# Performance work log

Hardware: AMD Instinct MI355X
Metric: run time of the kernel (lower is better)

## Reference

```python
import jax, jax.numpy as jnp
import numpy as np

B, T_ENC, T_DEC = 16, 256, 200
E, ATT, PRE, H, MEL, LOC, K = 512, 128, 256, 1024, 80, 32, 31


def setup_inputs() -> dict:
    key = jax.random.key(0)
    ks = jax.random.split(key, 20)
    s = lambda k, shape: jax.random.normal(k, shape, jnp.float32) * 0.02
    return dict(
        encoder_output=jax.random.normal(ks[0], (B, T_ENC, E), jnp.float32),
        padded_mels=jax.random.normal(ks[1], (B, T_DEC, MEL), jnp.float32),
        enc_proj_w=s(ks[2], (ATT, E)),
        lstm_proj_w=s(ks[3], (ATT, H)),
        loc_conv_w=s(ks[4], (LOC, 1, K)),
        loc_conv_b=jnp.zeros((LOC,), jnp.float32),
        loc_dense_w=s(ks[5], (ATT, LOC)),
        loc_dense_b=jnp.zeros((ATT,), jnp.float32),
        e_w=s(ks[6], (1, ATT)),
        e_b=jnp.zeros((1,), jnp.float32),
        prenet1_w=s(ks[7], (PRE, MEL)),
        prenet2_w=s(ks[8], (PRE, PRE)),
        w_ih0=s(ks[9], (4 * H, PRE + E)),
        w_hh0=s(ks[10], (4 * H, H)),
        b_ih0=jnp.zeros((4 * H,), jnp.float32),
        b_hh0=jnp.zeros((4 * H,), jnp.float32),
        w_ih1=s(ks[11], (4 * H, H)),
        w_hh1=s(ks[12], (4 * H, H)),
        b_ih1=jnp.zeros((4 * H,), jnp.float32),
        b_hh1=jnp.zeros((4 * H,), jnp.float32),
        proj_w=s(ks[13], (MEL, H + E)),
        proj_b=jnp.zeros((MEL,), jnp.float32),
        stop_w=s(ks[14], (1, H + E)),
        stop_b=jnp.zeros((1,), jnp.float32),
        text_lengths=jax.random.randint(ks[15], (B,), T_ENC // 2, T_ENC + 1),
    )


def _lstm_cell_zero(x, w_ih, b_ih, b_hh):
    # PyTorch LSTM cell with zero initial (h, c): h_prev contributes nothing
    # except the recurrent bias b_hh. Gate order: i, f, g, o.
    g = x @ w_ih.T + b_ih + b_hh
    i, f, gg, o = jnp.split(g, 4, axis=-1)
    c = jax.nn.sigmoid(i) * jnp.tanh(gg)  # f * c_prev == 0
    return jax.nn.sigmoid(o) * jnp.tanh(c)


def reference(encoder_output, padded_mels, enc_proj_w, lstm_proj_w, loc_conv_w,
              loc_conv_b, loc_dense_w, loc_dense_b, e_w, e_b, prenet1_w,
              prenet2_w, w_ih0, w_hh0, b_ih0, b_hh0, w_ih1, w_hh1, b_ih1,
              b_hh1, proj_w, proj_b, stop_w, stop_b, text_lengths):
    b, t_enc, _ = encoder_output.shape
    n_mel = padded_mels.shape[-1]
    h = w_hh0.shape[-1]
    pad = (loc_conv_w.shape[-1] - 1) // 2
    proc_enc = encoder_output @ enc_proj_w.T              # [B,Te,128]
    mask = jnp.arange(t_enc)[None, :] < text_lengths[:, None]
    # teacher forcing (ratio=1.0): prev mel at step t is padded_mels[:, t-1]
    prev_mels = jnp.concatenate(
        [jnp.zeros((b, 1, n_mel), padded_mels.dtype), padded_mels[:, :-1]],
        axis=1).transpose(1, 0, 2)                        # [Td,B,80]

    def step(carry, prev_mel):
        awc, h2 = carry                                   # [B,Te], [B,1024]
        # prenet (dropout omitted for a deterministic reference)
        x = jax.nn.relu(prev_mel @ prenet1_w.T)
        x = jax.nn.relu(x @ prenet2_w.T)                  # [B,256]
        # location-sensitive attention
        q = h2 @ lstm_proj_w.T                            # [B,128]
        loc = jax.lax.conv_general_dilated(
            awc[:, None, :], loc_conv_w, (1,), [(pad, pad)],
            dimension_numbers=('NCH', 'OIH', 'NCH')) + loc_conv_b[None, :, None]
        loc = jnp.einsum('bct,ac->bta', loc, loc_dense_w) + loc_dense_b
        en = jnp.tanh(q[:, None, :] + loc + proc_enc) @ e_w[0] + e_b[0]
        en = jnp.where(mask, en, -1e9)
        aw = jax.nn.softmax(en, axis=-1)                  # [B,Te]
        ctx = jnp.einsum('bt,bte->be', aw, encoder_output)  # [B,512]
        # 2-layer LSTM, state reset to zero every step (as in the original)
        li = jnp.concatenate([x, ctx], axis=-1)           # [B,768]
        h1 = _lstm_cell_zero(li, w_ih0, b_ih0, b_hh0)
        h2n = _lstm_cell_zero(h1, w_ih1, b_ih1, b_hh1)
        dec = jnp.concatenate([h2n, ctx], axis=-1)        # [B,1536]
        mel = dec @ proj_w.T + proj_b                     # [B,80]
        stop = (dec @ stop_w.T + stop_b)[:, 0]            # [B]
        return (awc + aw, h2n), (mel, stop)

    init = (jnp.zeros((b, t_enc), encoder_output.dtype),
            jnp.zeros((b, h), encoder_output.dtype))
    _, (mels, stops) = jax.lax.scan(step, init, prev_mels)
    return mels.transpose(1, 0, 2), stops.T               # [B,Td,80], [B,Td]
```

## Files before the change

kernel.cpp:

```cpp
#include <hip/hip_runtime.h>
#include <math.h>

#define NB   16
#define TE   256
#define TD   200
#define EE   512
#define ATT  128
#define PREN 256
#define HH   1024
#define NMEL 80
#define NLOC 32
#define KWW  31
#define PADW 15

#define OFF_X2H  0
#define OFF_PE   (OFF_X2H + TD*NB*128)
#define OFF_ENR  (OFF_PE + NB*TE*ATT)
#define OFF_CTR  (OFF_ENR + NB*16*6*4)
#define OFF_H1H  (OFF_CTR + NB*128*4)
#define OFF_H2R  (OFF_H1H + NB*512)
#define OFF_QVR  (OFF_H2R + NB*256*4)
#define OFF_BAR  (OFF_QVR + NB*16*2*4)
#define BAR_U32  4096
#define ARR_G 0

#define LW0X_U32 (12*128)
#define LW0C_U32 (12*256)
#define LW1_U32  (12*512)
#define DYN_BYTES ((LW0X_U32 + LW0C_U32 + LW1_U32)*4)

typedef float f4 __attribute__((ext_vector_type(4)));
typedef unsigned int u32x4 __attribute__((ext_vector_type(4)));
typedef unsigned int u32x2 __attribute__((ext_vector_type(2)));
typedef _Float16 h2t __attribute__((ext_vector_type(2)));

__device__ __forceinline__ float fast_sigm(float x) { return 1.0f / (1.0f + __expf(-x)); }
__device__ __forceinline__ float fast_tanh(float x) { return 1.0f - 2.0f / (__expf(2.0f*x) + 1.0f); }
__device__ __forceinline__ float dot4(f4 a, f4 b) {
  return a.x*b.x + a.y*b.y + a.z*b.z + a.w*b.w;
}
__device__ __forceinline__ float red32(float v) {
  v += __shfl_down(v, 16, 32); v += __shfl_down(v, 8, 32);
  v += __shfl_down(v, 4, 32);  v += __shfl_down(v, 2, 32);
  v += __shfl_down(v, 1, 32);
  return v;
}
__device__ __forceinline__ float red64(float v) {
  v += __shfl_down(v, 32); v += __shfl_down(v, 16); v += __shfl_down(v, 8);
  v += __shfl_down(v, 4);  v += __shfl_down(v, 2);  v += __shfl_down(v, 1);
  return v;
}
__device__ __forceinline__ float fdot2(unsigned a, unsigned b, float c) {
  return __builtin_amdgcn_fdot2(__builtin_bit_cast(h2t, a),
                                __builtin_bit_cast(h2t, b), c, false);
}
__device__ __forceinline__ unsigned pkh(float a, float b) {
  h2t h; h.x = (_Float16)a; h.y = (_Float16)b;
  return __builtin_bit_cast(unsigned, h);
}
__device__ __forceinline__ float hlo(unsigned u) {
  return (float)__builtin_bit_cast(h2t, u).x;
}
__device__ __forceinline__ float hhi(unsigned u) {
  return (float)__builtin_bit_cast(h2t, u).y;
}

__device__ __forceinline__ unsigned ld_cg_u32(const unsigned* p) {
  unsigned r;
  asm volatile("global_load_dword %0, %1, off sc0 sc1\n\ts_waitcnt vmcnt(0)"
               : "=v"(r) : "v"(p) : "memory");
  return r;
}
__device__ __forceinline__ void st_cg_u32(unsigned* p, unsigned v) {
  asm volatile("global_store_dword %0, %1, off sc0 sc1" :: "v"(p), "v"(v) : "memory");
}
__device__ __forceinline__ f4 ld_cg_f4(const f4* p) {
  f4 r;
  asm volatile("global_load_dwordx4 %0, %1, off sc0 sc1\n\ts_waitcnt vmcnt(0)"
               : "=v"(r) : "v"(p) : "memory");
  return r;
}
__device__ __forceinline__ void st_cg_f4(f4* p, f4 v) {
  asm volatile("global_store_dwordx4 %0, %1, off sc0 sc1" :: "v"(p), "v"(v) : "memory");
}
__device__ __forceinline__ u32x4 ld_cg_u4(const void* p) {
  u32x4 r;
  asm volatile("global_load_dwordx4 %0, %1, off sc0 sc1\n\ts_waitcnt vmcnt(0)"
               : "=v"(r) : "v"(p) : "memory");
  return r;
}
__device__ __forceinline__ void st_cg_u4(void* p, u32x4 v) {
  asm volatile("global_store_dwordx4 %0, %1, off sc0 sc1" :: "v"(p), "v"(v) : "memory");
}
__device__ __forceinline__ void st_cg_u2(void* p, u32x2 v) {
  asm volatile("global_store_dwordx2 %0, %1, off sc0 sc1" :: "v"(p), "v"(v) : "memory");
}
__device__ __forceinline__ f4 ld_l2_f4(const f4* p) {
  f4 r;
  asm volatile("global_load_dwordx4 %0, %1, off sc0\n\ts_waitcnt vmcnt(0)"
               : "=v"(r) : "v"(p) : "memory");
  return r;
}
__device__ __forceinline__ void st_l2_f4(f4* p, f4 v) {
  asm volatile("global_store_dwordx4 %0, %1, off sc0" :: "v"(p), "v"(v) : "memory");
}
__device__ __forceinline__ u32x4 ld_l2_u4(const void* p) {
  u32x4 r;
  asm volatile("global_load_dwordx4 %0, %1, off sc0\n\ts_waitcnt vmcnt(0)"
               : "=v"(r) : "v"(p) : "memory");
  return r;
}
__device__ __forceinline__ void st_l2_u4(void* p, u32x4 v) {
  asm volatile("global_store_dwordx4 %0, %1, off sc0" :: "v"(p), "v"(v) : "memory");
}
__device__ __forceinline__ void ld4u(u32x4& a, u32x4& b, u32x4& c, u32x4& d,
                                     const void* pa, const void* pb,
                                     const void* pc, const void* pd) {
  asm volatile(
    "global_load_dwordx4 %0, %4, off sc0 sc1\n\t"
    "global_load_dwordx4 %1, %5, off sc0 sc1\n\t"
    "global_load_dwordx4 %2, %6, off sc0 sc1\n\t"
    "global_load_dwordx4 %3, %7, off sc0 sc1\n\t"
    "s_waitcnt vmcnt(0)"
    : "=&v"(a), "=&v"(b), "=&v"(c), "=&v"(d)
    : "v"(pa), "v"(pb), "v"(pc), "v"(pd) : "memory");
}

__device__ __forceinline__ void g_arrive(unsigned* bar, unsigned e) {
  __syncthreads();
  if (threadIdx.x == 0) st_cg_u32(bar + ARR_G + blockIdx.x * 16, e);
}
__device__ __forceinline__ void g_wait(unsigned* bar, unsigned e) {
  if (threadIdx.x < 256) {
    while (ld_cg_u32(bar + ARR_G + threadIdx.x * 16) < e) {}
  }
  __syncthreads();
}

__global__ void k_init(float* __restrict__ ws) {
  const int gid = blockIdx.x * 256 + threadIdx.x;
  f4* enr = (f4*)(ws + OFF_ENR);
  u32x4* ctr = (u32x4*)(ws + OFF_CTR);
  f4* h2r = (f4*)(ws + OFF_H2R);
  f4* qvr = (f4*)(ws + OFF_QVR);
  unsigned* bar = (unsigned*)(ws + OFF_BAR);
  const f4 z = (f4){0.f, 0.f, 0.f, 0.f};
  const u32x4 zu = (u32x4){0u, 0u, 0u, 0u};
  for (int i = gid; i < NB*16*6; i += 32*256) st_cg_f4(enr + i, z);
  for (int i = gid; i < NB*128; i += 32*256) st_cg_u4(ctr + i, zu);
  for (int i = gid; i < NB*256; i += 32*256) st_cg_f4(h2r + i, z);
  for (int i = gid; i < NB*32; i += 32*256) st_cg_f4(qvr + i, z);
  for (int i = gid; i < BAR_U32; i += 32*256) st_cg_u32(bar + i, 0u);
}

__global__ void k_prenet(const float* __restrict__ mels,
                         const float* __restrict__ w1,
                         const float* __restrict__ w2,
                         float* __restrict__ ws) {
  const int t = blockIdx.x >> 4;
  const int b = blockIdx.x & 15;
  const int j = threadIdx.x;
  __shared__ float s_in[NMEL];
  __shared__ float s_x1[PREN];
  if (j < NMEL) s_in[j] = (t == 0) ? 0.0f : mels[(b*TD + (t-1))*NMEL + j];
  __syncthreads();
  float a1 = 0.0f;
  #pragma unroll 8
  for (int k = 0; k < NMEL; ++k) a1 += s_in[k] * w1[j*NMEL + k];
  s_x1[j] = fmaxf(a1, 0.0f);
  __syncthreads();
  float a2 = 0.0f;
  #pragma unroll 8
  for (int k = 0; k < PREN; ++k) a2 += s_x1[k] * w2[j*PREN + k];
  ((_Float16*)(ws + OFF_X2H))[((size_t)t*NB + b)*256 + j] = (_Float16)fmaxf(a2, 0.0f);
}

__global__ void k_procenc(const float* __restrict__ enc,
                          const float* __restrict__ w,
                          float* __restrict__ pe) {
  const int bt = blockIdx.x;
  const int a = threadIdx.x;
  __shared__ float s_e[EE];
  for (int k = a; k < EE; k += 128) s_e[k] = enc[bt*EE + k];
  __syncthreads();
  float acc = 0.0f;
  #pragma unroll 8
  for (int k = 0; k < EE; ++k) acc += s_e[k] * w[a*EE + k];
  pe[bt*ATT + a] = acc;
}

__global__ void __launch_bounds__(512, 1) k_main(
    const float* __restrict__ enc,
    const float* __restrict__ lstm_proj_w,
    const float* __restrict__ loc_conv_w,
    const float* __restrict__ loc_conv_b,
    const float* __restrict__ loc_dense_w,
    const float* __restrict__ loc_dense_b,
    const float* __restrict__ e_w,
    const float* __restrict__ e_b,
    const float* __restrict__ w_ih0,
    const float* __restrict__ b_ih0,
    const float* __restrict__ b_hh0,
    const float* __restrict__ w_ih1,
    const float* __restrict__ b_ih1,
    const float* __restrict__ b_hh1,
    const float* __restrict__ proj_w,
    const float* __restrict__ proj_b,
    const float* __restrict__ stop_w,
    const float* __restrict__ stop_b,
    const int*   __restrict__ text_len,
    float* __restrict__ ws,
    float* __restrict__ out) {
  const int bid = blockIdx.x;
  const int tid = threadIdx.x;

  const unsigned* x2h = (const unsigned*)(ws + OFF_X2H);
  float* pe  = ws + OFF_PE;
  f4* en_rec = (f4*)(ws + OFF_ENR);
  u32x4* ct_rec = (u32x4*)(ws + OFF_CTR);
  unsigned* h1h = (unsigned*)(ws + OFF_H1H);
  f4* h2_rec = (f4*)(ws + OFF_H2R);
  f4* qv_rec = (f4*)(ws + OFF_QVR);
  unsigned* bar = (unsigned*)(ws + OFF_BAR);

  __shared__ __align__(16) float s_ldw[NLOC*ATT];
  __shared__ float s_awcf[TE];
  __shared__ float s_loc[16*33];
  __shared__ float s_red[16];
  __shared__ float s_en[256];
  __shared__ float s_aw[256];
  __shared__ float s_entmp[16];
  __shared__ float s_qtmp[8];
  __shared__ float s_ctmp[32];
  __shared__ __align__(16) float s_q[ATT];
  __shared__ __align__(16) float s_dec[HH+EE];
  __shared__ float s_b0[12], s_b1[12];
  extern __shared__ __align__(16) unsigned dynlds_u[];
  unsigned* lw0x = dynlds_u;
  unsigned* lw0c = lw0x + LW0X_U32;
  unsigned* lw1  = lw0c + LW0C_U32;

  const int b_grp = bid & 15;
  const int sub   = bid >> 4;
  const int h0    = bid * 4;

  for (int i = tid; i < NLOC*ATT; i += 512) {
    int c = i >> 7, a = i & 127;
    s_ldw[i] = loc_dense_w[a*NLOC + c];
  }
  if (tid < 12) {
    int g = tid >> 2, h = tid & 3;
    int gr = (g == 0 ? 0 : (g == 1 ? 2048 : 3072)) + h0 + h;
    s_b0[tid] = b_ih0[gr] + b_hh0[gr];
    s_b1[tid] = b_ih1[gr] + b_hh1[gr];
  }
  for (int i = tid; i < LW0X_U32; i += 512) {
    int r = i >> 7, c = i & 127;
    int g = r >> 2, h = r & 3;
    int grow = (g == 0 ? 0 : (g == 1 ? 2048 : 3072)) + h0 + h;
    const float* wr = w_ih0 + (size_t)grow*768;
    lw0x[i] = pkh(wr[2*c], wr[2*c+1]);
  }
  for (int i = tid; i < LW0C_U32; i += 512) {
    int r = i >> 8, c = i & 255;
    int g = r >> 2, h = r & 3;
    int grow = (g == 0 ? 0 : (g == 1 ? 2048 : 3072)) + h0 + h;
    const float* wr = w_ih0 + (size_t)grow*768 + 256;
    lw0c[i] = pkh(wr[2*c], wr[2*c+1]);
  }
  for (int i = tid; i < LW1_U32; i += 512) {
    int r = i >> 9, c = i & 511;
    int g = r >> 2, h = r & 3;
    int grow = (g == 0 ? 0 : (g == 1 ? 2048 : 3072)) + h0 + h;
    const float* wr = w_ih1 + (size_t)grow*1024;
    lw1[i] = pkh(wr[2*c], wr[2*c+1]);
  }
  if (tid < 256) s_awcf[tid] = 0.0f;

  const int   lenb = text_len[b_grp];
  const float eb0  = e_b[0];
  const int tl = tid >> 5;
  const int j  = tid & 31;
  float lcw_r[KWW];
  #pragma unroll
  for (int k = 0; k < KWW; ++k) lcw_r[k] = loc_conv_w[j*KWW + k];
  const float lcb_r = loc_conv_b[j];
  const f4 db_r = *(const f4*)(loc_dense_b + 4*j);
  const f4 ew_r = *(const f4*)(e_w + 4*j);
  const f4 pe_r = *(const f4*)(pe + (size_t)(b_grp*TE + sub*16 + tl)*ATT + 4*j);
  const f4 ps_r = pe_r + db_r;
  const int e4i = tid >> 6;
  const int ts  = tid & 63;
  f4 encr[4];
  {
    const f4* enc4 = (const f4*)(enc + (size_t)b_grp*TE*EE);
    #pragma unroll
    for (int i = 0; i < 4; ++i)
      encr[i] = enc4[(size_t)(ts + 64*i)*(EE/4) + sub*8 + e4i];
  }
  const int en_si = tid / 6;
  const int en_rr = tid - en_si*6;
  const f4* en_myrec = en_rec + (b_grp*16 + en_si)*6 + en_rr;
  const int pb = tid >> 5;
  const int kc = tid & 31;
  const u32x4* ct_my = ct_rec + pb*128;
  __syncthreads();

  unsigned eg = 0;

  for (int t = 0; t < TD; ++t) {
    const unsigned tg = (unsigned)(t + 1);
    f4 pre;
    {
      float cv = lcb_r;
      const int pos = sub*16 + tl;
      #pragma unroll
      for (int k = 0; k < KWW; ++k) {
        const int g = pos - PADW + k;
        const float av = (g >= 0 && g < TE) ? s_awcf[g] : 0.0f;
        cv += av * lcw_r[k];
      }
      s_loc[tl*33 + j] = cv;
      __syncthreads();
      f4 d4 = (f4){0.f, 0.f, 0.f, 0.f};
      #pragma unroll 8
      for (int c = 0; c < NLOC; ++c) {
        const float lv = s_loc[tl*33 + c];
        const f4 w4 = ((const f4*)s_ldw)[c*32 + j];
        d4.x += lv*w4.x; d4.y += lv*w4.y; d4.z += lv*w4.z; d4.w += lv*w4.w;
      }
      pre = ps_r + d4;
    }
    {
      if (tid < 32) {
        const int src = tid >> 1, r = tid & 1;
        const f4* qp = qv_rec + (b_grp*16 + src)*2 + r;
        f4 v = ld_l2_f4(qp);
        while (__float_as_uint(v.z) != (unsigned)t) v = ld_cg_f4(qp);
        const unsigned u0 = __float_as_uint(v.x), u1 = __float_as_uint(v.y);
        const int base = src*8 + r*4;
        s_q[base+0] = hlo(u0); s_q[base+1] = hhi(u0);
        s_q[base+2] = hlo(u1); s_q[base+3] = hhi(u1);
      }
      __syncthreads();
      const f4 q4 = *(const f4*)(s_q + 4*j);
      float acc = fast_tanh(pre.x+q4.x)*ew_r.x + fast_tanh(pre.y+q4.y)*ew_r.y
                + fast_tanh(pre.z+q4.z)*ew_r.z + fast_tanh(pre.w+q4.w)*ew_r.w;
      acc = red32(acc);
      if (j == 0) {
        float evv = acc + eb0;
        const int tt = sub*16 + tl;
        if (tt >= lenb) evv = -1e9f;
        s_entmp[tl] = evv;
      }
      __syncthreads();
      if (tid < 6) {
        f4 r = (f4){0.f, 0.f, 0.f, __uint_as_float(tg)};
        const int base = 3*tid;
        r.x = s_entmp[base];
        if (base + 1 < 16) r.y = s_entmp[base+1];
        if (base + 2 < 16) r.z = s_entmp[base+2];
        f4* dst = en_rec + (b_grp*16 + sub)*6 + tid;
        st_l2_f4(dst, r);
        st_cg_f4(dst, r);
      }
    }
    {
      if (tid < 96) {
        f4 v = ld_l2_f4(en_myrec);
        while (__float_as_uint(v.w) != tg) v = ld_cg_f4(en_myrec);
        const int base = en_si*16 + 3*en_rr;
        s_en[base] = v.x;
        if (3*en_rr + 1 < 16) s_en[base+1] = v.y;
        if (3*en_rr + 2 < 16) s_en[base+2] = v.z;
      } else if (t > 0 && tid >= 128 && tid < 320) {
        const int ol = (tid - 128) >> 5, kq = tid & 31;
        const int m = sub*6 + ol;
        if (m < 81) {
          const float* wrow = (m < NMEL) ? (proj_w + (size_t)m*(HH+EE)) : stop_w;
          const f4* w4 = (const f4*)wrow;
          const f4* s4 = (const f4*)s_dec;
          float a2 = 0.0f;
          #pragma unroll
          for (int i = 0; i < 12; ++i) a2 += dot4(s4[kq + 32*i], w4[kq + 32*i]);
          a2 = red32(a2);
          if (kq == 0) {
            if (m < NMEL) out[(b_grp*TD + (t-1))*NMEL + m] = a2 + proj_b[m];
            else          out[NB*TD*NMEL + b_grp*TD + (t-1)] = a2 + stop_b[0];
          }
        }
      }
      __syncthreads();
      float p = 0.f;
      if (tid < 256) {
        p = __expf(s_en[tid]);
        float sm = p;
        #pragma unroll
        for (int d = 32; d > 0; d >>= 1) sm += __shfl_xor(sm, d);
        if ((tid & 63) == 0) s_red[8 + (tid >> 6)] = sm;
      }
      __syncthreads();
      const float inv = 1.0f / (s_red[8] + s_red[9] + s_red[10] + s_red[11]);
      if (tid < 256) {
        const float aw = p * inv;
        s_aw[tid] = aw;
        s_awcf[tid] += aw;
      }
      __syncthreads();
      f4 a4 = (f4){0.f, 0.f, 0.f, 0.f};
      #pragma unroll
      for (int i = 0; i < 4; ++i) {
        const float awv = s_aw[ts + 64*i];
        a4.x += awv*encr[i].x; a4.y += awv*encr[i].y;
        a4.z += awv*encr[i].z; a4.w += awv*encr[i].w;
      }
      a4.x = red64(a4.x); a4.y = red64(a4.y); a4.z = red64(a4.z); a4.w = red64(a4.w);
      if (ts == 0) {
        s_ctmp[e4i*4+0] = a4.x; s_ctmp[e4i*4+1] = a4.y;
        s_ctmp[e4i*4+2] = a4.z; s_ctmp[e4i*4+3] = a4.w;
      }
      __syncthreads();
      if (tid < 8) {
        u32x4 w;
        w.x = pkh(s_ctmp[4*tid+0], s_ctmp[4*tid+1]);
        w.y = pkh(s_ctmp[4*tid+2], s_ctmp[4*tid+3]);
        w.z = tg; w.w = 0u;
        u32x4* dst = ct_rec + b_grp*128 + sub*8 + tid;
        st_l2_u4(dst, w);
        st_cg_u4(dst, w);
      }
    }
    float acc[12];
    {
      #pragma unroll
      for (int r = 0; r < 12; ++r) acc[r] = 0.0f;
      const u32x4 xv = ((const u32x4*)x2h)[((size_t)t*NB + pb)*32 + kc];
      #pragma unroll
      for (int r = 0; r < 12; ++r) {
        const u32x4 w = ((const u32x4*)lw0x)[r*32 + kc];
        acc[r] = fdot2(xv.x, w.x, acc[r]); acc[r] = fdot2(xv.y, w.y, acc[r]);
        acc[r] = fdot2(xv.z, w.z, acc[r]); acc[r] = fdot2(xv.w, w.w, acc[r]);
      }
    }
    {
      u32x4 ra, rb, rc, rd;
      for (;;) {
        ld4u(ra, rb, rc, rd, ct_my + 2*kc, ct_my + 2*kc + 1,
             ct_my + 2*kc + 64, ct_my + 2*kc + 65);
        if (ra.z == tg && rb.z == tg && rc.z == tg && rd.z == tg) break;
        __builtin_amdgcn_s_sleep(1);
      }
      const u32x4 c0 = (u32x4){ra.x, ra.y, rb.x, rb.y};
      const u32x4 c1 = (u32x4){rc.x, rc.y, rd.x, rd.y};
      #pragma unroll
      for (int r = 0; r < 12; ++r) {
        const u32x4 w0 = ((const u32x4*)lw0c)[r*64 + kc];
        const u32x4 w1 = ((const u32x4*)lw0c)[r*64 + kc + 32];
        acc[r] = fdot2(c0.x, w0.x, acc[r]); acc[r] = fdot2(c0.y, w0.y, acc[r]);
        acc[r] = fdot2(c0.z, w0.z, acc[r]); acc[r] = fdot2(c0.w, w0.w, acc[r]);
        acc[r] = fdot2(c1.x, w1.x, acc[r]); acc[r] = fdot2(c1.y, w1.y, acc[r]);
        acc[r] = fdot2(c1.z, w1.z, acc[r]); acc[r] = fdot2(c1.w, w1.w, acc[r]);
      }
      #pragma unroll
      for (int r = 0; r < 12; ++r) acc[r] = red32(acc[r]);
      if (kc == 0) {
        float hv[4];
        #pragma unroll
        for (int h = 0; h < 4; ++h) {
          const float gi = acc[h]   + s_b0[h];
          const float gg = acc[4+h] + s_b0[4+h];
          const float go = acc[8+h] + s_b0[8+h];
          hv[h] = fast_sigm(go) * fast_tanh(fast_sigm(gi) * fast_tanh(gg));
        }
        u32x2 stv; stv.x = pkh(hv[0], hv[1]); stv.y = pkh(hv[2], hv[3]);
        st_cg_u2((u32x2*)h1h + pb*256 + bid, stv);
      }
    }
    g_arrive(bar, ++eg);
    g_wait(bar, eg);
    {
      #pragma unroll
      for (int r = 0; r < 12; ++r) acc[r] = 0.0f;
      u32x4 v0, v1, v2, v3;
      const u32x4* hp = (const u32x4*)h1h + pb*128 + kc;
      ld4u(v0, v1, v2, v3, hp, hp+32, hp+64, hp+96);
      #pragma unroll
      for (int r = 0; r < 12; ++r) {
        const u32x4* wp = (const u32x4*)lw1 + r*128 + kc;
        const u32x4 w0 = wp[0], w1 = wp[32], w2 = wp[64], w3 = wp[96];
        acc[r] = fdot2(v0.x, w0.x, acc[r]); acc[r] = fdot2(v0.y, w0.y, acc[r]);
        acc[r] = fdot2(v0.z, w0.z, acc[r]); acc[r] = fdot2(v0.w, w0.w, acc[r]);
        acc[r] = fdot2(v1.x, w1.x, acc[r]); acc[r] = fdot2(v1.y, w1.y, acc[r]);
        acc[r] = fdot2(v1.z, w1.z, acc[r]); acc[r] = fdot2(v1.w, w1.w, acc[r]);
        acc[r] = fdot2(v2.x, w2.x, acc[r]); acc[r] = fdot2(v2.y, w2.y, acc[r]);
        acc[r] = fdot2(v2.z, w2.z, acc[r]); acc[r] = fdot2(v2.w, w2.w, acc[r]);
        acc[r] = fdot2(v3.x, w3.x, acc[r]); acc[r] = fdot2(v3.y, w3.y, acc[r]);
        acc[r] = fdot2(v3.z, w3.z, acc[r]); acc[r] = fdot2(v3.w, w3.w, acc[r]);
      }
      #pragma unroll
      for (int r = 0; r < 12; ++r) acc[r] = red32(acc[r]);
      if (kc == 0) {
        float hv[4];
        #pragma unroll
        for (int h = 0; h < 4; ++h) {
          const float gi = acc[h]   + s_b1[h];
          const float gg = acc[4+h] + s_b1[4+h];
          const float go = acc[8+h] + s_b1[8+h];
          hv[h] = fast_sigm(go) * fast_tanh(fast_sigm(gi) * fast_tanh(gg));
        }
        f4 r;
        r.x = __uint_as_float(pkh(hv[0], hv[1]));
        r.y = __uint_as_float(pkh(hv[2], hv[3]));
        r.z = __uint_as_float(tg); r.w = 0.f;
        st_cg_f4(h2_rec + pb*256 + bid, r);
      }
    }
    {
      if (tid < 256) {
        const f4* hp = h2_rec + b_grp*256 + tid;
        f4 v;
        do { v = ld_cg_f4(hp); } while (__float_as_uint(v.z) != tg);
        const unsigned u0 = __float_as_uint(v.x), u1 = __float_as_uint(v.y);
        s_dec[4*tid+0] = hlo(u0); s_dec[4*tid+1] = hhi(u0);
        s_dec[4*tid+2] = hlo(u1); s_dec[4*tid+3] = hhi(u1);
      } else if (tid < 384) {
        const int i = tid - 256;
        const u32x4* cp = ct_rec + b_grp*128 + i;
        u32x4 v = ld_l2_u4(cp);
        while (v.z != tg) v = ld_cg_u4(cp);
        s_dec[HH + 4*i + 0] = hlo(v.x); s_dec[HH + 4*i + 1] = hhi(v.x);
        s_dec[HH + 4*i + 2] = hlo(v.y); s_dec[HH + 4*i + 3] = hhi(v.y);
      }
      __syncthreads();
      const int row = tid >> 6;
      const int kq  = tid & 63;
      const int a   = sub*8 + row;
      const f4* w4 = (const f4*)(lstm_proj_w + (size_t)a*HH);
      const f4* s4 = (const f4*)s_dec;
      float a2 = 0.0f;
      #pragma unroll
      for (int i = 0; i < 4; ++i) a2 += dot4(s4[kq + 64*i], w4[kq + 64*i]);
      a2 = red64(a2);
      if (kq == 0) s_qtmp[row] = a2;
      __syncthreads();
      if (tid < 2) {
        f4 r;
        r.x = __uint_as_float(pkh(s_qtmp[4*tid+0], s_qtmp[4*tid+1]));
        r.y = __uint_as_float(pkh(s_qtmp[4*tid+2], s_qtmp[4*tid+3]));
        r.z = __uint_as_float(tg); r.w = 0.f;
        f4* dst = qv_rec + (b_grp*16 + sub)*2 + tid;
        st_l2_f4(dst, r);
        st_cg_f4(dst, r);
      }
    }
  }
  __syncthreads();
  {
    const int ol = tid >> 5, kq = tid & 31;
    if (ol < 6) {
      const int m = sub*6 + ol;
      if (m < 81) {
        const float* wrow = (m < NMEL) ? (proj_w + (size_t)m*(HH+EE)) : stop_w;
        const f4* w4 = (const f4*)wrow;
        const f4* s4 = (const f4*)s_dec;
        float a2 = 0.0f;
        #pragma unroll
        for (int i = 0; i < 12; ++i) a2 += dot4(s4[kq + 32*i], w4[kq + 32*i]);
        a2 = red32(a2);
        if (kq == 0) {
          if (m < NMEL) out[(b_grp*TD + (TD-1))*NMEL + m] = a2 + proj_b[m];
          else          out[NB*TD*NMEL + b_grp*TD + (TD-1)] = a2 + stop_b[0];
        }
      }
    }
  }
}

extern "C" void kernel_launch(void* const* d_in, const int* in_sizes, int n_in,
                              void* d_out, int out_size, void* d_ws, size_t ws_size,
                              hipStream_t stream) {
  (void)in_sizes; (void)n_in; (void)out_size; (void)ws_size;
  const float* enc         = (const float*)d_in[0];
  const float* mels        = (const float*)d_in[1];
  const float* enc_proj_w  = (const float*)d_in[2];
  const float* lstm_proj_w = (const float*)d_in[3];
  const float* loc_conv_w  = (const float*)d_in[4];
  const float* loc_conv_b  = (const float*)d_in[5];
  const float* loc_dense_w = (const float*)d_in[6];
  const float* loc_dense_b = (const float*)d_in[7];
  const float* e_w         = (const float*)d_in[8];
  const float* e_b         = (const float*)d_in[9];
  const float* prenet1_w   = (const float*)d_in[10];
  const float* prenet2_w   = (const float*)d_in[11];
  const float* w_ih0       = (const float*)d_in[12];
  const float* b_ih0       = (const float*)d_in[14];
  const float* b_hh0       = (const float*)d_in[15];
  const float* w_ih1       = (const float*)d_in[16];
  const float* b_ih1       = (const float*)d_in[18];
  const float* b_hh1       = (const float*)d_in[19];
  const float* proj_w      = (const float*)d_in[20];
  const float* proj_b      = (const float*)d_in[21];
  const float* stop_w      = (const float*)d_in[22];
  const float* stop_b      = (const float*)d_in[23];
  const int*   text_len    = (const int*)d_in[24];
  float* ws  = (float*)d_ws;
  float* out = (float*)d_out;

  static int attr_set = 0;
  if (!attr_set) {
    hipFuncSetAttribute((const void*)k_main,
                        hipFuncAttributeMaxDynamicSharedMemorySize, DYN_BYTES);
    attr_set = 1;
  }

  k_init<<<dim3(32), dim3(256), 0, stream>>>(ws);
  k_prenet<<<dim3(TD*NB), dim3(256), 0, stream>>>(mels, prenet1_w, prenet2_w, ws);
  k_procenc<<<dim3(NB*TE), dim3(128), 0, stream>>>(enc, enc_proj_w, ws + OFF_PE);

  k_main<<<dim3(256), dim3(512), DYN_BYTES, stream>>>(
      enc, lstm_proj_w, loc_conv_w, loc_conv_b, loc_dense_w, loc_dense_b,
      e_w, e_b, w_ih0, b_ih0, b_hh0, w_ih1, b_ih1, b_hh1,
      proj_w, proj_b, stop_w, stop_b, text_len, ws, out);
}
```

Baseline: 3.719 ms.

## Compute attention query redundantly per block, removing cross-block query exchange

```diff
diff --git a/kernel.cpp b/kernel.cpp
--- a/kernel.cpp
+++ b/kernel.cpp
@@ -19,8 +19,7 @@
 #define OFF_CTR  (OFF_ENR + NB*16*6*4)
 #define OFF_H1H  (OFF_CTR + NB*128*4)
 #define OFF_H2R  (OFF_H1H + NB*512)
-#define OFF_QVR  (OFF_H2R + NB*256*4)
-#define OFF_BAR  (OFF_QVR + NB*16*2*4)
+#define OFF_BAR  (OFF_H2R + NB*256*4)
 #define BAR_U32  4096
 #define ARR_G 0
 
@@ -142,14 +141,12 @@
   f4* enr = (f4*)(ws + OFF_ENR);
   u32x4* ctr = (u32x4*)(ws + OFF_CTR);
   f4* h2r = (f4*)(ws + OFF_H2R);
-  f4* qvr = (f4*)(ws + OFF_QVR);
   unsigned* bar = (unsigned*)(ws + OFF_BAR);
   const f4 z = (f4){0.f, 0.f, 0.f, 0.f};
   const u32x4 zu = (u32x4){0u, 0u, 0u, 0u};
   for (int i = gid; i < NB*16*6; i += 32*256) st_cg_f4(enr + i, z);
   for (int i = gid; i < NB*128; i += 32*256) st_cg_u4(ctr + i, zu);
   for (int i = gid; i < NB*256; i += 32*256) st_cg_f4(h2r + i, z);
-  for (int i = gid; i < NB*32; i += 32*256) st_cg_f4(qvr + i, z);
   for (int i = gid; i < BAR_U32; i += 32*256) st_cg_u32(bar + i, 0u);
 }
 
@@ -220,7 +217,6 @@
   u32x4* ct_rec = (u32x4*)(ws + OFF_CTR);
   unsigned* h1h = (unsigned*)(ws + OFF_H1H);
   f4* h2_rec = (f4*)(ws + OFF_H2R);
-  f4* qv_rec = (f4*)(ws + OFF_QVR);
   unsigned* bar = (unsigned*)(ws + OFF_BAR);
 
   __shared__ __align__(16) float s_ldw[NLOC*ATT];
@@ -230,7 +226,6 @@
   __shared__ float s_en[256];
   __shared__ float s_aw[256];
   __shared__ float s_entmp[16];
-  __shared__ float s_qtmp[8];
   __shared__ float s_ctmp[32];
   __shared__ __align__(16) float s_q[ATT];
   __shared__ __align__(16) float s_dec[HH+EE];
@@ -301,6 +296,9 @@
   const int en_si = tid / 6;
   const int en_rr = tid - en_si*6;
   const f4* en_myrec = en_rec + (b_grp*16 + en_si)*6 + en_rr;
+  const int qa = tid >> 2;
+  const int qk = tid & 3;
+  const f4* wq4 = (const f4*)(lstm_proj_w + (size_t)qa*HH);
   const int pb = tid >> 5;
   const int kc = tid & 31;
   const u32x4* ct_my = ct_rec + pb*128;
@@ -332,17 +330,33 @@
       pre = ps_r + d4;
     }
     {
-      if (tid < 32) {
-        const int src = tid >> 1, r = tid & 1;
-        const f4* qp = qv_rec + (b_grp*16 + src)*2 + r;
-        f4 v = ld_l2_f4(qp);
-        while (__float_as_uint(v.z) != (unsigned)t) v = ld_cg_f4(qp);
+      const unsigned tgp = (unsigned)t;
+      if (tid < 256) {
+        const f4* hp = h2_rec + b_grp*256 + tid;
+        f4 v;
+        do { v = ld_cg_f4(hp); } while (__float_as_uint(v.z) != tgp);
         const unsigned u0 = __float_as_uint(v.x), u1 = __float_as_uint(v.y);
-        const int base = src*8 + r*4;
-        s_q[base+0] = hlo(u0); s_q[base+1] = hhi(u0);
-        s_q[base+2] = hlo(u1); s_q[base+3] = hhi(u1);
-      }
-      __syncthreads();
+        s_dec[4*tid+0] = hlo(u0); s_dec[4*tid+1] = hhi(u0);
+        s_dec[4*tid+2] = hlo(u1); s_dec[4*tid+3] = hhi(u1);
+      } else if (tid < 384) {
+        const int i = tid - 256;
+        const u32x4* cp = ct_rec + b_grp*128 + i;
+        u32x4 v = ld_l2_u4(cp);
+        while (v.z != tgp) v = ld_cg_u4(cp);
+        s_dec[HH + 4*i + 0] = hlo(v.x); s_dec[HH + 4*i + 1] = hhi(v.x);
+        s_dec[HH + 4*i + 2] = hlo(v.y); s_dec[HH + 4*i + 3] = hhi(v.y);
+      }
+      __syncthreads();
+      const f4* s4 = (const f4*)s_dec;
+      float a2 = 0.0f;
+      #pragma unroll 8
+      for (int i = 0; i < 64; ++i) a2 += dot4(s4[qk + 4*i], wq4[qk + 4*i]);
+      a2 += __shfl_down(a2, 2, 4);
+      a2 += __shfl_down(a2, 1, 4);
+      if (qk == 0) s_q[qa] = a2;
+      __syncthreads();
+    }
+    {
       const f4 q4 = *(const f4*)(s_q + 4*j);
       float acc = fast_tanh(pre.x+q4.x)*ew_r.x + fast_tanh(pre.y+q4.y)*ew_r.y
                 + fast_tanh(pre.z+q4.z)*ew_r.z + fast_tanh(pre.w+q4.w)*ew_r.w;
@@ -515,47 +529,25 @@
         st_cg_f4(h2_rec + pb*256 + bid, r);
       }
     }
-    {
-      if (tid < 256) {
-        const f4* hp = h2_rec + b_grp*256 + tid;
-        f4 v;
-        do { v = ld_cg_f4(hp); } while (__float_as_uint(v.z) != tg);
-        const unsigned u0 = __float_as_uint(v.x), u1 = __float_as_uint(v.y);
-        s_dec[4*tid+0] = hlo(u0); s_dec[4*tid+1] = hhi(u0);
-        s_dec[4*tid+2] = hlo(u1); s_dec[4*tid+3] = hhi(u1);
-      } else if (tid < 384) {
-        const int i = tid - 256;
-        const u32x4* cp = ct_rec + b_grp*128 + i;
-        u32x4 v = ld_l2_u4(cp);
-        while (v.z != tg) v = ld_cg_u4(cp);
-        s_dec[HH + 4*i + 0] = hlo(v.x); s_dec[HH + 4*i + 1] = hhi(v.x);
-        s_dec[HH + 4*i + 2] = hlo(v.y); s_dec[HH + 4*i + 3] = hhi(v.y);
-      }
-      __syncthreads();
-      const int row = tid >> 6;
-      const int kq  = tid & 63;
-      const int a   = sub*8 + row;
-      const f4* w4 = (const f4*)(lstm_proj_w + (size_t)a*HH);
-      const f4* s4 = (const f4*)s_dec;
-      float a2 = 0.0f;
-      #pragma unroll
-      for (int i = 0; i < 4; ++i) a2 += dot4(s4[kq + 64*i], w4[kq + 64*i]);
-      a2 = red64(a2);
-      if (kq == 0) s_qtmp[row] = a2;
-      __syncthreads();
-      if (tid < 2) {
-        f4 r;
-        r.x = __uint_as_float(pkh(s_qtmp[4*tid+0], s_qtmp[4*tid+1]));
-        r.y = __uint_as_float(pkh(s_qtmp[4*tid+2], s_qtmp[4*tid+3]));
-        r.z = __uint_as_float(tg); r.w = 0.f;
-        f4* dst = qv_rec + (b_grp*16 + sub)*2 + tid;
-        st_l2_f4(dst, r);
-        st_cg_f4(dst, r);
-      }
-    }
-  }
-  __syncthreads();
+  }
   {
+    const unsigned tgf = (unsigned)TD;
+    if (tid < 256) {
+      const f4* hp = h2_rec + b_grp*256 + tid;
+      f4 v;
+      do { v = ld_cg_f4(hp); } while (__float_as_uint(v.z) != tgf);
+      const unsigned u0 = __float_as_uint(v.x), u1 = __float_as_uint(v.y);
+      s_dec[4*tid+0] = hlo(u0); s_dec[4*tid+1] = hhi(u0);
+      s_dec[4*tid+2] = hlo(u1); s_dec[4*tid+3] = hhi(u1);
+    } else if (tid < 384) {
+      const int i = tid - 256;
+      const u32x4* cp = ct_rec + b_grp*128 + i;
+      u32x4 v = ld_l2_u4(cp);
+      while (v.z != tgf) v = ld_cg_u4(cp);
+      s_dec[HH + 4*i + 0] = hlo(v.x); s_dec[HH + 4*i + 1] = hhi(v.x);
+      s_dec[HH + 4*i + 2] = hlo(v.y); s_dec[HH + 4*i + 3] = hhi(v.y);
+    }
+    __syncthreads();
     const int ol = tid >> 5, kq = tid & 31;
     if (ol < 6) {
       const int m = sub*6 + ol;
```

Result: slower. 4.751 ms (+27.8%).

## Compute next step's location conv and LSTM0 input dot during grid barrier wait

Applied to the files above, without the earlier changes.

```diff
diff --git a/kernel.cpp b/kernel.cpp
--- a/kernel.cpp
+++ b/kernel.cpp
@@ -307,30 +307,41 @@
   __syncthreads();
 
   unsigned eg = 0;
+  f4 pre;
+  float xacc[12];
+
+  {
+    float cv = lcb_r;
+    const int pos = sub*16 + tl;
+    #pragma unroll
+    for (int k = 0; k < KWW; ++k) {
+      const int g = pos - PADW + k;
+      const float av = (g >= 0 && g < TE) ? s_awcf[g] : 0.0f;
+      cv += av * lcw_r[k];
+    }
+    s_loc[tl*33 + j] = cv;
+    __syncthreads();
+    f4 d4 = (f4){0.f, 0.f, 0.f, 0.f};
+    #pragma unroll 8
+    for (int c = 0; c < NLOC; ++c) {
+      const float lv = s_loc[tl*33 + c];
+      const f4 w4 = ((const f4*)s_ldw)[c*32 + j];
+      d4.x += lv*w4.x; d4.y += lv*w4.y; d4.z += lv*w4.z; d4.w += lv*w4.w;
+    }
+    pre = ps_r + d4;
+    #pragma unroll
+    for (int r = 0; r < 12; ++r) xacc[r] = 0.0f;
+    const u32x4 xv = ((const u32x4*)x2h)[(size_t)pb*32 + kc];
+    #pragma unroll
+    for (int r = 0; r < 12; ++r) {
+      const u32x4 w = ((const u32x4*)lw0x)[r*32 + kc];
+      xacc[r] = fdot2(xv.x, w.x, xacc[r]); xacc[r] = fdot2(xv.y, w.y, xacc[r]);
+      xacc[r] = fdot2(xv.z, w.z, xacc[r]); xacc[r] = fdot2(xv.w, w.w, xacc[r]);
+    }
+  }
 
   for (int t = 0; t < TD; ++t) {
     const unsigned tg = (unsigned)(t + 1);
-    f4 pre;
-    {
-      float cv = lcb_r;
-      const int pos = sub*16 + tl;
-      #pragma unroll
-      for (int k = 0; k < KWW; ++k) {
-        const int g = pos - PADW + k;
-        const float av = (g >= 0 && g < TE) ? s_awcf[g] : 0.0f;
-        cv += av * lcw_r[k];
-      }
-      s_loc[tl*33 + j] = cv;
-      __syncthreads();
-      f4 d4 = (f4){0.f, 0.f, 0.f, 0.f};
-      #pragma unroll 8
-      for (int c = 0; c < NLOC; ++c) {
-        const float lv = s_loc[tl*33 + c];
-        const f4 w4 = ((const f4*)s_ldw)[c*32 + j];
-        d4.x += lv*w4.x; d4.y += lv*w4.y; d4.z += lv*w4.z; d4.w += lv*w4.w;
-      }
-      pre = ps_r + d4;
-    }
     {
       if (tid < 32) {
         const int src = tid >> 1, r = tid & 1;
@@ -430,19 +441,10 @@
         st_cg_u4(dst, w);
       }
     }
-    float acc[12];
     {
-      #pragma unroll
-      for (int r = 0; r < 12; ++r) acc[r] = 0.0f;
-      const u32x4 xv = ((const u32x4*)x2h)[((size_t)t*NB + pb)*32 + kc];
-      #pragma unroll
-      for (int r = 0; r < 12; ++r) {
-        const u32x4 w = ((const u32x4*)lw0x)[r*32 + kc];
-        acc[r] = fdot2(xv.x, w.x, acc[r]); acc[r] = fdot2(xv.y, w.y, acc[r]);
-        acc[r] = fdot2(xv.z, w.z, acc[r]); acc[r] = fdot2(xv.w, w.w, acc[r]);
-      }
-    }
-    {
+      float acc[12];
+      #pragma unroll
+      for (int r = 0; r < 12; ++r) acc[r] = xacc[r];
       u32x4 ra, rb, rc, rd;
       for (;;) {
         ld4u(ra, rb, rc, rd, ct_my + 2*kc, ct_my + 2*kc + 1,
@@ -477,8 +479,38 @@
       }
     }
     g_arrive(bar, ++eg);
+    if (t + 1 < TD) {
+      float cv = lcb_r;
+      const int pos = sub*16 + tl;
+      #pragma unroll
+      for (int k = 0; k < KWW; ++k) {
+        const int g = pos - PADW + k;
+        const float av = (g >= 0 && g < TE) ? s_awcf[g] : 0.0f;
+        cv += av * lcw_r[k];
+      }
+      s_loc[tl*33 + j] = cv;
+      __syncthreads();
+      f4 d4 = (f4){0.f, 0.f, 0.f, 0.f};
+      #pragma unroll 8
+      for (int c = 0; c < NLOC; ++c) {
+        const float lv = s_loc[tl*33 + c];
+        const f4 w4 = ((const f4*)s_ldw)[c*32 + j];
+        d4.x += lv*w4.x; d4.y += lv*w4.y; d4.z += lv*w4.z; d4.w += lv*w4.w;
+      }
+      pre = ps_r + d4;
+      #pragma unroll
+      for (int r = 0; r < 12; ++r) xacc[r] = 0.0f;
+      const u32x4 xv = ((const u32x4*)x2h)[((size_t)(t+1)*NB + pb)*32 + kc];
+      #pragma unroll
+      for (int r = 0; r < 12; ++r) {
+        const u32x4 w = ((const u32x4*)lw0x)[r*32 + kc];
+        xacc[r] = fdot2(xv.x, w.x, xacc[r]); xacc[r] = fdot2(xv.y, w.y, xacc[r]);
+        xacc[r] = fdot2(xv.z, w.z, xacc[r]); xacc[r] = fdot2(xv.w, w.w, xacc[r]);
+      }
+    }
     g_wait(bar, eg);
     {
+      float acc[12];
       #pragma unroll
       for (int r = 0; r < 12; ++r) acc[r] = 0.0f;
       u32x4 v0, v1, v2, v3;
```

New measurement: 4.156 ms. 1.12x slower.
